# Optimization experiments

Hardware: AMD Instinct MI355X
Metric: run time of the kernel (lower is better)

Reference implementation:

```python
import jax, jax.numpy as jnp
import numpy as np

WIN, SHIFT, HEADS = 12, 6, 24

def _rel_index(win):
    coords = np.stack(np.meshgrid(np.arange(win), np.arange(win), indexing='ij'))  # [2,w,w]
    flat = coords.reshape(2, -1)
    rel = (flat[:, :, None] - flat[:, None, :]).transpose(1, 2, 0).astype(np.int64)  # [N,N,2]
    rel[..., 0] += win - 1
    rel[..., 1] += win - 1
    rel[..., 0] *= 2 * win - 1
    return rel.sum(-1).reshape(-1).astype(np.int32)  # [N*N]

def _shift_mask(H, W, win, shift, dtype):
    img = np.zeros((H, W), np.float32)
    cnt = 0
    for hs in (slice(0, -win), slice(-win, -shift), slice(-shift, None)):
        for ws in (slice(0, -win), slice(-win, -shift), slice(-shift, None)):
            img[hs, ws] = cnt
            cnt += 1
    mw = img.reshape(H // win, win, W // win, win).transpose(0, 2, 1, 3).reshape(-1, win * win)  # [nW,N]
    diff = mw[:, None, :] - mw[:, :, None]
    return jnp.asarray(np.where(diff != 0, -100.0, 0.0), dtype=dtype)  # [nW,N,N]

def setup_inputs() -> dict:
    key = jax.random.key(0)
    ks = jax.random.split(key, 5)
    B, H, W, C = 64, 24, 24, 768
    x = jax.random.normal(ks[0], (B, H, W, C), jnp.float32)
    qkv_w = jax.random.normal(ks[1], (C, 3 * C), jnp.float32) * 0.02
    qkv_b = jnp.zeros((3 * C,), jnp.float32)
    proj_w = jax.random.normal(ks[2], (C, C), jnp.float32) * 0.02
    proj_b = jnp.zeros((C,), jnp.float32)
    rpb_table = jax.random.normal(ks[3], ((2 * WIN - 1) ** 2, HEADS), jnp.float32) * 0.02
    rel_index = jnp.asarray(_rel_index(WIN))
    return {"x": x, "qkv_w": qkv_w, "qkv_b": qkv_b, "proj_w": proj_w,
            "proj_b": proj_b, "rpb_table": rpb_table, "rel_index": rel_index}

def reference(x, qkv_w, qkv_b, proj_w, proj_b, rpb_table, rel_index):
    B, H, W, C = x.shape
    win, shift, heads = WIN, SHIFT, HEADS
    d = C // heads
    scale = d ** -0.5
    N = win * win
    nWh, nWw = H // win, W // win
    nW = nWh * nWw
    # cyclic shift
    xs = jnp.roll(x, (-shift, -shift), axis=(1, 2))
    # window partition -> [B*nW, N, C]
    xw = xs.reshape(B, nWh, win, nWw, win, C).transpose(0, 1, 3, 2, 4, 5).reshape(B * nW, N, C)
    qkv = (xw @ qkv_w + qkv_b).reshape(B * nW, N, 3, heads, d).transpose(2, 0, 3, 1, 4)
    q, k, v = qkv[0] * scale, qkv[1], qkv[2]  # [B*nW, h, N, d]
    attn = jnp.einsum('bhnd,bhmd->bhnm', q, k)
    bias = rpb_table[rel_index].reshape(N, N, heads).transpose(2, 0, 1)  # [h,N,N]
    attn = attn + bias[None]
    mask = _shift_mask(H, W, win, shift, attn.dtype)  # [nW,N,N], static
    attn = (attn.reshape(B, nW, heads, N, N) + mask[None, :, None]).reshape(B * nW, heads, N, N)
    attn = jax.nn.softmax(attn, axis=-1)
    out = jnp.einsum('bhnm,bhmd->bhnd', attn, v).transpose(0, 2, 1, 3).reshape(B * nW, N, C)
    out = out @ proj_w + proj_b
    # window merge + reverse shift
    out = out.reshape(B, nWh, nWw, win, win, C).transpose(0, 1, 3, 2, 4, 5).reshape(B, H, W, C)
    out = jnp.roll(out, (shift, shift), axis=(1, 2))
    # L2 normalize over channel dim (L2N)
    return out / jnp.sqrt(jnp.sum(out * out, axis=-1, keepdims=True) + 1e-6)
```

## Files before the change

kernel.cpp:

```cpp
#include <hip/hip_runtime.h>

typedef unsigned short u16;
typedef __bf16 bf16x8 __attribute__((ext_vector_type(8)));
typedef float f32x4 __attribute__((ext_vector_type(4)));
typedef u16 u16x8 __attribute__((ext_vector_type(8)));
typedef u16 u16x4 __attribute__((ext_vector_type(4)));

__device__ __forceinline__ u16 f2bf(float f) {
    union { float f; unsigned u; } v; v.f = f;
    unsigned r = v.u + 0x7FFFu + ((v.u >> 16) & 1u);
    return (u16)(r >> 16);
}

#define AS1 __attribute__((address_space(1)))
#define AS3 __attribute__((address_space(3)))
__device__ __forceinline__ void gload_lds16(const void* g, void* l) {
    __builtin_amdgcn_global_load_lds((const AS1 void*)(g), (AS3 void*)(l), 16, 0, 0);
}


__global__ __launch_bounds__(256) void prep_x_kernel(const float* __restrict__ x, u16* __restrict__ xw) {
    unsigned i = ((unsigned)blockIdx.x * 256u + threadIdx.x) * 4u;
    int R = (int)(i / 768u); int c = (int)(i % 768u);
    int w = R / 144, nn = R - w * 144;
    int b = w >> 2, wi = w & 3;
    int r = nn / 12, cc = nn - r * 12;
    int sh = (wi >> 1) * 12 + r + 6; if (sh >= 24) sh -= 24;
    int sw = (wi & 1) * 12 + cc + 6; if (sw >= 24) sw -= 24;
    const float* src = x + (((size_t)b * 24 + sh) * 24 + sw) * 768 + c;
    f32x4 v = *(const f32x4*)src;
    u16x4 o; o[0] = f2bf(v[0]); o[1] = f2bf(v[1]); o[2] = f2bf(v[2]); o[3] = f2bf(v[3]);
    size_t idx = ((size_t)(R >> 7) * 24 + (c >> 5)) * 4096 + (R & 127) * 32 + (c & 31);
    *(u16x4*)(xw + idx) = o;
}

__global__ __launch_bounds__(256) void transpose_cast_kernel(const float* __restrict__ w, u16* __restrict__ wt,
                                                             int K, int N) {
    __shared__ float tile[32][33];
    int tx = threadIdx.x & 31, ty = threadIdx.x >> 5;
    int nb = blockIdx.x * 32, kb = blockIdx.y * 32;
#pragma unroll
    for (int rr = 0; rr < 32; rr += 8) tile[rr + ty][tx] = w[(size_t)(kb + rr + ty) * N + nb + tx];
    __syncthreads();
#pragma unroll
    for (int rr = 0; rr < 32; rr += 8) {
        int n = nb + rr + ty, k = kb + tx;
        wt[((size_t)(n >> 7) * 24 + (k >> 5)) * 4096 + (n & 127) * 32 + (k & 31)] = f2bf(tile[tx][rr + ty]);
    }
}

__global__ __launch_bounds__(256) void make_bias_kernel(const float* __restrict__ tab, const int* __restrict__ rel,
                                                        float* __restrict__ bm) {
    int i = blockIdx.x * 256 + threadIdx.x;
    int h = i / 20736, nm = i - h * 20736;
    bm[i] = tab[rel[nm] * 24 + h];
}

#define FENCE asm volatile("" ::: "memory")
#define BARRIER __builtin_amdgcn_s_barrier()

#define STAGE_TILE(gp, ldsoff)                                                                 \
    { const char* srcb = (const char*)(gp);                                                    \
      _Pragma("unroll") for (int j = 0; j < 2; j++) {                                          \
        int off = j * 4096 + t * 16;                                                           \
        gload_lds16(srcb + off, (char*)lds + (ldsoff) + off);                                  \
    } }

template <int EPI>
__global__ __launch_bounds__(256, 3) void gemm128_kernel(const u16* __restrict__ A, const u16* __restrict__ Bt,
                                                         const float* __restrict__ bias,
                                                         u16* __restrict__ o0, u16* __restrict__ o1, u16* __restrict__ o2,
                                                         float* __restrict__ of, int Ndim, int Kdim, int nxb, float qscale) {
    __shared__ __align__(16) u16 lds[24576];
    const int t = threadIdx.x, lane = t & 63, wv = t >> 6;
    const int wr = wv >> 1, wc = wv & 1;
    const int l15 = lane & 15, lg = lane >> 4;
    int nwg = gridDim.x, orig = blockIdx.x;
    int q = nwg >> 3, r = nwg & 7, xcd = orig & 7, loc = orig >> 3;
    int wg = (xcd < r ? xcd * (q + 1) : r * (q + 1) + (xcd - r) * q) + loc;
    int by = wg / nxb, bx = wg - by * nxb;
    const int bm = by << 7, bn = bx << 7;

    f32x4 acc[4][4] = {};
    const int NT = Kdim >> 5;
    const u16* Ap = A + (size_t)(bm >> 7) * NT * 4096;
    const u16* Bp = Bt + (size_t)(bn >> 7) * NT * 4096;

    STAGE_TILE(Ap, 0);
    STAGE_TILE(Bp, 8192);
    STAGE_TILE(Ap + 4096, 16384);
    STAGE_TILE(Bp + 4096, 16384 + 8192);
    asm volatile("s_waitcnt vmcnt(4)" ::: "memory");
    FENCE; BARRIER;

    int ba = 0;
    for (int T = 0; T < NT; ++T) {
        const char* rb = (const char*)lds + ba * 16384;
        char* sb = (char*)lds + (ba >= 1 ? ba - 1 : 2) * 16384;
        if (T + 2 < NT) {
            STAGE_TILE(Ap + (T + 2) * 4096, sb - (char*)lds);
            STAGE_TILE(Bp + (T + 2) * 4096, sb - (char*)lds + 8192);
        }
        bf16x8 aR[4], bR[4];
#pragma unroll
        for (int mf = 0; mf < 4; mf++)
            aR[mf] = *(const bf16x8*)(rb + (wr * 64 + mf * 16 + l15) * 64 + lg * 16);
#pragma unroll
        for (int nf = 0; nf < 4; nf++)
            bR[nf] = *(const bf16x8*)(rb + 8192 + (wc * 64 + nf * 16 + l15) * 64 + lg * 16);
        __builtin_amdgcn_s_setprio(1);
#pragma unroll
        for (int mf = 0; mf < 4; mf++)
#pragma unroll
            for (int nf = 0; nf < 4; nf++)
                acc[mf][nf] = __builtin_amdgcn_mfma_f32_16x16x32_bf16(aR[mf], bR[nf], acc[mf][nf], 0, 0, 0);
        __builtin_amdgcn_s_setprio(0);
        if (T + 2 < NT)      { asm volatile("s_waitcnt vmcnt(4)" ::: "memory"); FENCE; BARRIER; }
        else if (T + 1 < NT) { asm volatile("s_waitcnt vmcnt(0)" ::: "memory"); FENCE; BARRIER; }
        ba = (ba == 2) ? 0 : ba + 1;
    }

#pragma unroll
    for (int mf = 0; mf < 4; mf++) {
        int Rbase = bm + wr * 64 + mf * 16 + lg * 4;
#pragma unroll
        for (int nf = 0; nf < 4; nf++) {
            int Cg = bn + wc * 64 + nf * 16 + l15;
            float bv = bias[Cg];
            if (EPI == 0) {
                int s = Cg / 768; int rem = Cg - s * 768; int h = rem >> 5; int dd = rem & 31;
#pragma unroll
                for (int rg = 0; rg < 4; rg++) {
                    int R = Rbase + rg;
                    int w2 = R / 144; int nn = R - w2 * 144;
                    float v = acc[mf][nf][rg] + bv;
                    if (s == 0)      o0[((size_t)(w2 * 24 + h) * 144 + nn) * 32 + dd] = f2bf(v * qscale);
                    else if (s == 1) o1[((size_t)(w2 * 24 + h) * 144 + nn) * 32 + dd] = f2bf(v);
                    else             o2[((size_t)(w2 * 24 + h) * 32 + dd) * 144 + nn] = f2bf(v);
                }
            } else {
#pragma unroll
                for (int rg = 0; rg < 4; rg++) {
                    int R = Rbase + rg;
                    of[(size_t)R * Ndim + Cg] = acc[mf][nf][rg] + bv;
                }
            }
        }
    }
}

__global__ __launch_bounds__(576) void attn_kernel(const u16* __restrict__ Qg, const u16* __restrict__ Kg,
                                                   const u16* __restrict__ Vg, const float* __restrict__ bias_mat,
                                                   u16* __restrict__ Ob) {
    __shared__ __align__(16) u16 Qs[144 * 40];
    __shared__ __align__(16) u16 Ks[144 * 40];
    __shared__ __align__(16) u16 Vs[32 * 160];
    __shared__ __align__(16) u16 Ps[144 * 160];
    const int bx = blockIdx.x;
    const int w = bx / 24, h = bx - w * 24;
    const int wi = w & 3, wh = wi >> 1, ww = wi & 1;
    const int t = threadIdx.x, lane = t & 63, wv = t >> 6;
    const int l15 = lane & 15, lg = lane >> 4;
    const size_t base = (size_t)bx * 4608;
    {
        int nn = t >> 2, dd = (t & 3) << 3;
        *(u16x8*)(Qs + nn * 40 + dd) = *(const u16x8*)(Qg + base + nn * 32 + dd);
        *(u16x8*)(Ks + nn * 40 + dd) = *(const u16x8*)(Kg + base + nn * 32 + dd);
        int rv = t / 18, cv = (t - rv * 18) * 8;
        int ba = (rv * 320 + cv * 2) ^ ((rv & 7) << 4);
        *(u16x8*)((char*)Vs + ba) = *(const u16x8*)(Vg + base + rv * 144 + cv);
    }
    u16x8 zz = (u16x8)0;
    if (t < 64)  { int rv = t >> 1, cv = 144 + (t & 1) * 8; int ba = (rv * 320 + cv * 2) ^ ((rv & 7) << 4); *(u16x8*)((char*)Vs + ba) = zz; }
    if (t < 288) { int rv = t >> 1, cv = 144 + (t & 1) * 8; int ba = (rv * 320 + cv * 2) ^ ((rv & 7) << 4); *(u16x8*)((char*)Ps + ba) = zz; }
    __syncthreads();

    f32x4 S[9];
    {
        bf16x8 aq = *(const bf16x8*)(Qs + (wv * 16 + l15) * 40 + lg * 8);
        f32x4 z4 = (f32x4)0.0f;
#pragma unroll
        for (int j = 0; j < 9; j++) {
            bf16x8 bk = *(const bf16x8*)(Ks + (j * 16 + l15) * 40 + lg * 8);
            S[j] = __builtin_amdgcn_mfma_f32_16x16x32_bf16(aq, bk, z4, 0, 0, 0);
        }
    }
    int regm[9];
#pragma unroll
    for (int j = 0; j < 9; j++) {
        int m = j * 16 + l15; int r = m / 12, c = m - r * 12;
        int rid = wh ? (r < 6 ? 1 : 2) : 0;
        int cid = ww ? (c < 6 ? 1 : 2) : 0;
        regm[j] = rid * 3 + cid;
    }
    const float* bh = bias_mat + h * 20736;
#pragma unroll
    for (int rg = 0; rg < 4; rg++) {
        int n = wv * 16 + lg * 4 + rg;
        int r = n / 12, c = n - r * 12;
        int rid = wh ? (r < 6 ? 1 : 2) : 0;
        int cid = ww ? (c < 6 ? 1 : 2) : 0;
        int regn = rid * 3 + cid;
        const float* bhn = bh + n * 144;
        float mx = -1e30f;
#pragma unroll
        for (int j = 0; j < 9; j++) {
            float v = S[j][rg] + bhn[j * 16 + l15];
            if (regn != regm[j]) v -= 100.0f;
            S[j][rg] = v;
            mx = fmaxf(mx, v);
        }
#pragma unroll
        for (int d = 1; d < 16; d <<= 1) mx = fmaxf(mx, __shfl_xor(mx, d));
        float sum = 0.0f;
#pragma unroll
        for (int j = 0; j < 9; j++) { float e = __expf(S[j][rg] - mx); S[j][rg] = e; sum += e; }
#pragma unroll
        for (int d = 1; d < 16; d <<= 1) sum += __shfl_xor(sum, d);
        float inv = 1.0f / sum;
#pragma unroll
        for (int j = 0; j < 9; j++) {
            int ba = (n * 320 + (j * 16 + l15) * 2) ^ ((n & 7) << 4);
            *(u16*)((char*)Ps + ba) = f2bf(S[j][rg] * inv);
        }
    }
    __syncthreads();
    f32x4 o0 = (f32x4)0.0f, o1 = (f32x4)0.0f;
#pragma unroll
    for (int ks = 0; ks < 5; ks++) {
        int k2 = (ks * 32 + lg * 8) * 2;
        int ra = wv * 16 + l15;
        bf16x8 ap = *(const bf16x8*)((char*)Ps + ((ra * 320 + k2) ^ ((ra & 7) << 4)));
        int rv0 = l15, rv1 = 16 + l15;
        bf16x8 b0 = *(const bf16x8*)((char*)Vs + ((rv0 * 320 + k2) ^ ((rv0 & 7) << 4)));
        bf16x8 b1 = *(const bf16x8*)((char*)Vs + ((rv1 * 320 + k2) ^ ((rv1 & 7) << 4)));
        o0 = __builtin_amdgcn_mfma_f32_16x16x32_bf16(ap, b0, o0, 0, 0, 0);
        o1 = __builtin_amdgcn_mfma_f32_16x16x32_bf16(ap, b1, o1, 0, 0, 0);
    }
#pragma unroll
    for (int rg = 0; rg < 4; rg++) {
        int n = wv * 16 + lg * 4 + rg;
        int R = w * 144 + n;
        size_t idx = ((size_t)(R >> 7) * 24 + h) * 4096 + (R & 127) * 32;
        Ob[idx + l15]      = f2bf(o0[rg]);
        Ob[idx + 16 + l15] = f2bf(o1[rg]);
    }
}

__global__ __launch_bounds__(256) void norm_kernel(const float* __restrict__ raw, float* __restrict__ out) {
    int R = blockIdx.x * 4 + (threadIdx.x >> 6);
    int lane = threadIdx.x & 63;
    const float* src = raw + (size_t)R * 768;
    f32x4 v0 = *(const f32x4*)(src + lane * 4);
    f32x4 v1 = *(const f32x4*)(src + lane * 4 + 256);
    f32x4 v2 = *(const f32x4*)(src + lane * 4 + 512);
    float ss = v0[0]*v0[0] + v0[1]*v0[1] + v0[2]*v0[2] + v0[3]*v0[3]
             + v1[0]*v1[0] + v1[1]*v1[1] + v1[2]*v1[2] + v1[3]*v1[3]
             + v2[0]*v2[0] + v2[1]*v2[1] + v2[2]*v2[2] + v2[3]*v2[3];
#pragma unroll
    for (int d = 1; d < 64; d <<= 1) ss += __shfl_xor(ss, d);
    float inv = 1.0f / sqrtf(ss + 1e-6f);
    int w = R / 144, nn = R - w * 144;
    int b = w >> 2, wi = w & 3;
    int r = nn / 12, cc = nn - r * 12;
    int oh = (wi >> 1) * 12 + r + 6; if (oh >= 24) oh -= 24;
    int ow = (wi & 1) * 12 + cc + 6; if (ow >= 24) ow -= 24;
    float* dst = out + (((size_t)b * 24 + oh) * 24 + ow) * 768;
    v0 *= inv; v1 *= inv; v2 *= inv;
    *(f32x4*)(dst + lane * 4) = v0;
    *(f32x4*)(dst + lane * 4 + 256) = v1;
    *(f32x4*)(dst + lane * 4 + 512) = v2;
}

extern "C" void kernel_launch(void* const* d_in, const int* in_sizes, int n_in,
                              void* d_out, int out_size, void* d_ws, size_t ws_size,
                              hipStream_t stream) {
    const float* x      = (const float*)d_in[0];
    const float* qkv_w  = (const float*)d_in[1];
    const float* qkv_b  = (const float*)d_in[2];
    const float* proj_w = (const float*)d_in[3];
    const float* proj_b = (const float*)d_in[4];
    const float* rpb    = (const float*)d_in[5];
    const int*   rel    = (const int*)d_in[6];

    char* ws = (char*)d_ws;
    const size_t SZ = 56623104;
    u16*   xw   = (u16*)(ws);
    u16*   Qb   = (u16*)(ws + SZ);
    u16*   Kb   = (u16*)(ws + 2 * SZ);
    u16*   Vt   = (u16*)(ws + 3 * SZ);
    u16*   Ob   = (u16*)(ws + 4 * SZ);
    u16*   qwt  = (u16*)(ws + 5 * SZ);
    u16*   pwt  = (u16*)(ws + 5 * SZ + 3538944);
    float* bm   = (float*)(ws + 5 * SZ + 3538944 + 1179648);
    float* raw  = (float*)(ws);

    prep_x_kernel<<<27648, 256, 0, stream>>>(x, xw);
    transpose_cast_kernel<<<dim3(72, 24), 256, 0, stream>>>(qkv_w, qwt, 768, 2304);
    transpose_cast_kernel<<<dim3(24, 24), 256, 0, stream>>>(proj_w, pwt, 768, 768);
    make_bias_kernel<<<1944, 256, 0, stream>>>(rpb, rel, bm);

    gemm128_kernel<0><<<5184, 256, 0, stream>>>(xw, qwt, qkv_b, Qb, Kb, Vt, nullptr,
                                                2304, 768, 18, 0.17677669529663687f);
    attn_kernel<<<6144, 576, 0, stream>>>(Qb, Kb, Vt, bm, Ob);
    gemm128_kernel<1><<<1728, 256, 0, stream>>>(Ob, pwt, proj_b, nullptr, nullptr, nullptr,
                                                raw, 768, 768, 6, 1.0f);
    norm_kernel<<<9216, 256, 0, stream>>>(raw, (float*)d_out);
}
```

Baseline: 473.5 us.

## Store bias and projection output in bf16, double-buffer GEMM for occupancy

The relative-position bias matrix and the projection GEMM output are now kept in bf16 instead of fp32, halving the traffic for bias reads in attention and for the raw output passed to the L2-normalize kernel. The GEMM drops from a three-stage to a two-stage LDS pipeline, cutting shared memory so launch bounds can request more resident blocks, at the cost of waiting on each tile load before the next iteration. The norm kernel is rewritten to read bf16 with a different lane-to-channel mapping. Rounding the pre-normalization output to bf16 adds precision error.

```diff
diff --git a/kernel.cpp b/kernel.cpp
--- a/kernel.cpp
+++ b/kernel.cpp
@@ -10,6 +10,9 @@
     union { float f; unsigned u; } v; v.f = f;
     unsigned r = v.u + 0x7FFFu + ((v.u >> 16) & 1u);
     return (u16)(r >> 16);
+}
+__device__ __forceinline__ float bf2f(u16 u) {
+    union { unsigned u; float f; } v; v.u = ((unsigned)u) << 16; return v.f;
 }
 
 #define AS1 __attribute__((address_space(1)))
@@ -50,10 +53,10 @@
 }
 
 __global__ __launch_bounds__(256) void make_bias_kernel(const float* __restrict__ tab, const int* __restrict__ rel,
-                                                        float* __restrict__ bm) {
+                                                        u16* __restrict__ bm) {
     int i = blockIdx.x * 256 + threadIdx.x;
     int h = i / 20736, nm = i - h * 20736;
-    bm[i] = tab[rel[nm] * 24 + h];
+    bm[i] = f2bf(tab[rel[nm] * 24 + h]);
 }
 
 #define FENCE asm volatile("" ::: "memory")
@@ -67,11 +70,11 @@
     } }
 
 template <int EPI>
-__global__ __launch_bounds__(256, 3) void gemm128_kernel(const u16* __restrict__ A, const u16* __restrict__ Bt,
+__global__ __launch_bounds__(256, 5) void gemm128_kernel(const u16* __restrict__ A, const u16* __restrict__ Bt,
                                                          const float* __restrict__ bias,
                                                          u16* __restrict__ o0, u16* __restrict__ o1, u16* __restrict__ o2,
-                                                         float* __restrict__ of, int Ndim, int Kdim, int nxb, float qscale) {
-    __shared__ __align__(16) u16 lds[24576];
+                                                         int Ndim, int Kdim, int nxb, float qscale) {
+    __shared__ __align__(16) u16 lds[16384];
     const int t = threadIdx.x, lane = t & 63, wv = t >> 6;
     const int wr = wv >> 1, wc = wv & 1;
     const int l15 = lane & 15, lg = lane >> 4;
@@ -88,18 +91,15 @@
 
     STAGE_TILE(Ap, 0);
     STAGE_TILE(Bp, 8192);
-    STAGE_TILE(Ap + 4096, 16384);
-    STAGE_TILE(Bp + 4096, 16384 + 8192);
-    asm volatile("s_waitcnt vmcnt(4)" ::: "memory");
+    asm volatile("s_waitcnt vmcnt(0)" ::: "memory");
     FENCE; BARRIER;
 
-    int ba = 0;
     for (int T = 0; T < NT; ++T) {
-        const char* rb = (const char*)lds + ba * 16384;
-        char* sb = (char*)lds + (ba >= 1 ? ba - 1 : 2) * 16384;
-        if (T + 2 < NT) {
-            STAGE_TILE(Ap + (T + 2) * 4096, sb - (char*)lds);
-            STAGE_TILE(Bp + (T + 2) * 4096, sb - (char*)lds + 8192);
+        const char* rb = (const char*)lds + (T & 1) * 16384;
+        const int nb = ((T + 1) & 1) * 16384;
+        if (T + 1 < NT) {
+            STAGE_TILE(Ap + (T + 1) * 4096, nb);
+            STAGE_TILE(Bp + (T + 1) * 4096, nb + 8192);
         }
         bf16x8 aR[4], bR[4];
 #pragma unroll
@@ -115,9 +115,10 @@
             for (int nf = 0; nf < 4; nf++)
                 acc[mf][nf] = __builtin_amdgcn_mfma_f32_16x16x32_bf16(aR[mf], bR[nf], acc[mf][nf], 0, 0, 0);
         __builtin_amdgcn_s_setprio(0);
-        if (T + 2 < NT)      { asm volatile("s_waitcnt vmcnt(4)" ::: "memory"); FENCE; BARRIER; }
-        else if (T + 1 < NT) { asm volatile("s_waitcnt vmcnt(0)" ::: "memory"); FENCE; BARRIER; }
-        ba = (ba == 2) ? 0 : ba + 1;
+        if (T + 1 < NT) {
+            asm volatile("s_waitcnt vmcnt(0)" ::: "memory");
+            FENCE; BARRIER;
+        }
     }
 
 #pragma unroll
@@ -142,7 +143,7 @@
 #pragma unroll
                 for (int rg = 0; rg < 4; rg++) {
                     int R = Rbase + rg;
-                    of[(size_t)R * Ndim + Cg] = acc[mf][nf][rg] + bv;
+                    o0[(size_t)R * Ndim + Cg] = f2bf(acc[mf][nf][rg] + bv);
                 }
             }
         }
@@ -150,7 +151,7 @@
 }
 
 __global__ __launch_bounds__(576) void attn_kernel(const u16* __restrict__ Qg, const u16* __restrict__ Kg,
-                                                   const u16* __restrict__ Vg, const float* __restrict__ bias_mat,
+                                                   const u16* __restrict__ Vg, const u16* __restrict__ bias_mat,
                                                    u16* __restrict__ Ob) {
     __shared__ __align__(16) u16 Qs[144 * 40];
     __shared__ __align__(16) u16 Ks[144 * 40];
@@ -193,7 +194,7 @@
         int cid = ww ? (c < 6 ? 1 : 2) : 0;
         regm[j] = rid * 3 + cid;
     }
-    const float* bh = bias_mat + h * 20736;
+    const u16* bh = bias_mat + h * 20736;
 #pragma unroll
     for (int rg = 0; rg < 4; rg++) {
         int n = wv * 16 + lg * 4 + rg;
@@ -201,11 +202,11 @@
         int rid = wh ? (r < 6 ? 1 : 2) : 0;
         int cid = ww ? (c < 6 ? 1 : 2) : 0;
         int regn = rid * 3 + cid;
-        const float* bhn = bh + n * 144;
+        const u16* bhn = bh + n * 144;
         float mx = -1e30f;
 #pragma unroll
         for (int j = 0; j < 9; j++) {
-            float v = S[j][rg] + bhn[j * 16 + l15];
+            float v = S[j][rg] + bf2f(bhn[j * 16 + l15]);
             if (regn != regm[j]) v -= 100.0f;
             S[j][rg] = v;
             mx = fmaxf(mx, v);
@@ -247,29 +248,35 @@
     }
 }
 
-__global__ __launch_bounds__(256) void norm_kernel(const float* __restrict__ raw, float* __restrict__ out) {
+__global__ __launch_bounds__(256) void norm_kernel(const u16* __restrict__ raw, float* __restrict__ out) {
     int R = blockIdx.x * 4 + (threadIdx.x >> 6);
     int lane = threadIdx.x & 63;
-    const float* src = raw + (size_t)R * 768;
-    f32x4 v0 = *(const f32x4*)(src + lane * 4);
-    f32x4 v1 = *(const f32x4*)(src + lane * 4 + 256);
-    f32x4 v2 = *(const f32x4*)(src + lane * 4 + 512);
-    float ss = v0[0]*v0[0] + v0[1]*v0[1] + v0[2]*v0[2] + v0[3]*v0[3]
-             + v1[0]*v1[0] + v1[1]*v1[1] + v1[2]*v1[2] + v1[3]*v1[3]
-             + v2[0]*v2[0] + v2[1]*v2[1] + v2[2]*v2[2] + v2[3]*v2[3];
+    const u16* src = raw + (size_t)R * 768;
+    u16x8 a = *(const u16x8*)(src + lane * 8);
+    u16x4 b = *(const u16x4*)(src + 512 + lane * 4);
+    float f[12];
+#pragma unroll
+    for (int k = 0; k < 8; k++) f[k] = bf2f(a[k]);
+#pragma unroll
+    for (int k = 0; k < 4; k++) f[8 + k] = bf2f(b[k]);
+    float ss = 0.0f;
+#pragma unroll
+    for (int k = 0; k < 12; k++) ss += f[k] * f[k];
 #pragma unroll
     for (int d = 1; d < 64; d <<= 1) ss += __shfl_xor(ss, d);
     float inv = 1.0f / sqrtf(ss + 1e-6f);
     int w = R / 144, nn = R - w * 144;
-    int b = w >> 2, wi = w & 3;
+    int bb = w >> 2, wi = w & 3;
     int r = nn / 12, cc = nn - r * 12;
     int oh = (wi >> 1) * 12 + r + 6; if (oh >= 24) oh -= 24;
     int ow = (wi & 1) * 12 + cc + 6; if (ow >= 24) ow -= 24;
-    float* dst = out + (((size_t)b * 24 + oh) * 24 + ow) * 768;
-    v0 *= inv; v1 *= inv; v2 *= inv;
-    *(f32x4*)(dst + lane * 4) = v0;
-    *(f32x4*)(dst + lane * 4 + 256) = v1;
-    *(f32x4*)(dst + lane * 4 + 512) = v2;
+    float* dst = out + (((size_t)bb * 24 + oh) * 24 + ow) * 768;
+    f32x4 v0, v1, v2;
+#pragma unroll
+    for (int k = 0; k < 4; k++) { v0[k] = f[k] * inv; v1[k] = f[4 + k] * inv; v2[k] = f[8 + k] * inv; }
+    *(f32x4*)(dst + lane * 8) = v0;
+    *(f32x4*)(dst + lane * 8 + 4) = v1;
+    *(f32x4*)(dst + 512 + lane * 4) = v2;
 }
 
 extern "C" void kernel_launch(void* const* d_in, const int* in_sizes, int n_in,
@@ -292,18 +299,18 @@
     u16*   Ob   = (u16*)(ws + 4 * SZ);
     u16*   qwt  = (u16*)(ws + 5 * SZ);
     u16*   pwt  = (u16*)(ws + 5 * SZ + 3538944);
-    float* bm   = (float*)(ws + 5 * SZ + 3538944 + 1179648);
-    float* raw  = (float*)(ws);
+    u16*   bm   = (u16*)(ws + 5 * SZ + 3538944 + 1179648);
+    u16*   raw16 = (u16*)(ws);
 
     prep_x_kernel<<<27648, 256, 0, stream>>>(x, xw);
     transpose_cast_kernel<<<dim3(72, 24), 256, 0, stream>>>(qkv_w, qwt, 768, 2304);
     transpose_cast_kernel<<<dim3(24, 24), 256, 0, stream>>>(proj_w, pwt, 768, 768);
     make_bias_kernel<<<1944, 256, 0, stream>>>(rpb, rel, bm);
 
-    gemm128_kernel<0><<<5184, 256, 0, stream>>>(xw, qwt, qkv_b, Qb, Kb, Vt, nullptr,
+    gemm128_kernel<0><<<5184, 256, 0, stream>>>(xw, qwt, qkv_b, Qb, Kb, Vt,
                                                 2304, 768, 18, 0.17677669529663687f);
     attn_kernel<<<6144, 576, 0, stream>>>(Qb, Kb, Vt, bm, Ob);
-    gemm128_kernel<1><<<1728, 256, 0, stream>>>(Ob, pwt, proj_b, nullptr, nullptr, nullptr,
-                                                raw, 768, 768, 6, 1.0f);
-    norm_kernel<<<9216, 256, 0, stream>>>(raw, (float*)d_out);
-}
+    gemm128_kernel<1><<<1728, 256, 0, stream>>>(Ob, pwt, proj_b, raw16, nullptr, nullptr,
+                                                768, 768, 6, 1.0f);
+    norm_kernel<<<9216, 256, 0, stream>>>(raw16, (float*)d_out);
+}
```

Result: slower. 859.6 us (+81.5%).
